# Performance work log

Hardware: AMD Instinct MI355X
Metric: run time of the kernel (lower is better)

Reference implementation:

```python
import jax, jax.numpy as jnp
import numpy as np

N = 8192          # bbox_num
C = 2048          # in_channels
IC = C // 2       # inter_channels


def setup_inputs() -> dict:
    key = jax.random.key(0)
    ks = jax.random.split(key, 12)
    s_lin = 1.0 / np.sqrt(C)    # torch Linear init scale for fan_in=C
    s_w = 1.0 / np.sqrt(IC)     # for fan_in=IC
    return {
        "x": jax.random.normal(ks[0], (N, C), dtype=jnp.float32),
        "theta_w": jax.random.uniform(ks[1], (IC, C), jnp.float32, -s_lin, s_lin),
        "theta_b": jax.random.uniform(ks[2], (IC,), jnp.float32, -s_lin, s_lin),
        "phi_w": jax.random.uniform(ks[3], (IC, C), jnp.float32, -s_lin, s_lin),
        "phi_b": jax.random.uniform(ks[4], (IC,), jnp.float32, -s_lin, s_lin),
        "g_w": jax.random.uniform(ks[5], (IC, C), jnp.float32, -s_lin, s_lin),
        "g_b": jax.random.uniform(ks[6], (IC,), jnp.float32, -s_lin, s_lin),
        "W_w": jax.random.uniform(ks[7], (C, IC), jnp.float32, -s_w, s_w),
        "W_b": jax.random.uniform(ks[8], (C,), jnp.float32, -s_w, s_w),
        "mask_w": jax.random.uniform(ks[9], (N, C), jnp.float32, -s_lin, s_lin),
        "mask_b": jax.random.uniform(ks[10], (N,), jnp.float32, -s_lin, s_lin),
    }


def reference(x, theta_w, theta_b, phi_w, phi_b, g_w, g_b, W_w, W_b, mask_w, mask_b):
    # x: [N, C]. torch Linear: y = x @ W^T + b
    g_x = x @ g_w.T + g_b              # [N, IC]
    theta_x = x @ theta_w.T + theta_b  # [N, IC]
    phi_x = x @ phi_w.T + phi_b        # [N, IC]
    f = theta_x @ phi_x.T              # [N, N]
    # resize(): ad-hoc Linear(C -> N) then softmax over last dim
    mask = jax.nn.softmax(x @ mask_w.T + mask_b, axis=-1)  # [N, N]
    f = f * mask
    f_div_C = jax.nn.softmax(f, axis=-1)  # [N, N]
    y = f_div_C @ g_x                  # [N, IC]
    W_y = y @ W_w.T + W_b              # [N, C]
    z = W_y + x                        # residual
    return (z, f_div_C)
```

## Files before the change

kernel.cpp:

```cpp
#include <hip/hip_runtime.h>
#include <hip/hip_bf16.h>

typedef __bf16 bf16_t;
typedef __bf16 bf16x8 __attribute__((ext_vector_type(8)));
typedef float f32x4 __attribute__((ext_vector_type(4)));

#define GLOAD16(gp, lp) __builtin_amdgcn_global_load_lds(                      \
    (const __attribute__((address_space(1))) void*)(gp),                       \
    (__attribute__((address_space(3))) void*)(lp), 16, 0, 0)
#define BARRIER() asm volatile("s_barrier" ::: "memory")
#define VMC(n) asm volatile("s_waitcnt vmcnt(" #n ")" ::: "memory")
#define LGK0()                                                                 \
  do {                                                                         \
    asm volatile("s_waitcnt lgkmcnt(0)" ::: "memory");                         \
    __builtin_amdgcn_sched_barrier(0);                                         \
  } while (0)

__global__ __launch_bounds__(256) void cast_f32_bf16_k(
    const float* __restrict__ in, bf16_t* __restrict__ out, long n8) {
  long i = (long)blockIdx.x * blockDim.x + threadIdx.x;
  long stride = (long)gridDim.x * blockDim.x;
  for (; i < n8; i += stride) {
    long e = i * 8;
    float4 a = *(const float4*)(in + e);
    float4 b = *(const float4*)(in + e + 4);
    bf16x8 o;
    o[0] = (__bf16)a.x; o[1] = (__bf16)a.y; o[2] = (__bf16)a.z; o[3] = (__bf16)a.w;
    o[4] = (__bf16)b.x; o[5] = (__bf16)b.y; o[6] = (__bf16)b.z; o[7] = (__bf16)b.w;
    *(bf16x8*)(out + e) = o;
  }
}

template <int BIAS, bool EMASK, bool RES, bool OUTBF16>
__global__ __launch_bounds__(512, 2) void gemm256(
    const bf16_t* __restrict__ A, long lda, const bf16_t* __restrict__ B,
    long ldb, const float* __restrict__ bias, const bf16_t* __restrict__ ml,
    const float* __restrict__ mrow, const float* __restrict__ invrow,
    const float* __restrict__ res, float* __restrict__ outf,
    bf16_t* __restrict__ outb, int M, int N, int K) {
  __shared__ __align__(1024) char lds[131072];
  const int tid = threadIdx.x;
  const int gx = N >> 8;
  int bid = blockIdx.y * gx + blockIdx.x;
  const int nwg = gridDim.x * gridDim.y;
  const int cpx = nwg >> 3;
  bid = (bid & 7) * cpx + (bid >> 3);
  const long row0 = (long)(bid / gx) * 256;
  const long col0 = (long)(bid % gx) * 256;

  const int w = tid >> 6, lane = tid & 63;
  const int wm = w >> 2, wn = w & 3;
  const int fr = lane & 15, fq = lane >> 4;

  const int arow = (wm * 128 + fr) * 128;
  const int brow = 32768 + (wn * 64 + fr) * 128;
  const int sw0 = ((fq ^ (fr & 7)) << 4);
  const int sw1 = (((4 | fq) ^ (fr & 7)) << 4);

  const int r0 = tid >> 3;
  const int s0 = (tid & 7) ^ (r0 & 7);
  const bf16_t* Ap = A + (row0 + r0) * lda + s0 * 8;
  const bf16_t* Bp = B + (col0 + r0) * ldb + s0 * 8;
  const int dstA = w * 1024;

#define STG_A(h, U)                                                            \
  {                                                                            \
    const bf16_t* s_ = Ap + (long)(h)*128 * lda + (long)(U)*64;                \
    char* d_ = lds + (((U)&1) * 65536) + (h)*16384 + dstA;                     \
    GLOAD16(s_, d_);                                                           \
    GLOAD16(s_ + 64 * lda, d_ + 8192);                                         \
  }
#define STG_B(h, U)                                                            \
  {                                                                            \
    const bf16_t* s_ = Bp + (long)(h)*128 * ldb + (long)(U)*64;                \
    char* d_ = lds + (((U)&1) * 65536) + 32768 + (h)*16384 + dstA;             \
    GLOAD16(s_, d_);                                                           \
    GLOAD16(s_ + 64 * ldb, d_ + 8192);                                         \
  }
#define RD_A(buf, s)                                                           \
  {                                                                            \
    _Pragma("unroll") for (int i = 0; i < 4; ++i) {                            \
      aS[i * 2] = *(const bf16x8*)((buf) + arow + ((s)*4 + i) * 2048 + sw0);   \
      aS[i * 2 + 1] =                                                          \
          *(const bf16x8*)((buf) + arow + ((s)*4 + i) * 2048 + sw1);           \
    }                                                                          \
  }
#define RD_B(dst, buf, s)                                                      \
  {                                                                            \
    _Pragma("unroll") for (int j = 0; j < 2; ++j) {                            \
      dst[j * 2] = *(const bf16x8*)((buf) + brow + ((s)*2 + j) * 2048 + sw0);  \
      dst[j * 2 + 1] =                                                         \
          *(const bf16x8*)((buf) + brow + ((s)*2 + j) * 2048 + sw1);           \
    }                                                                          \
  }
#define QUAD(BV, I0, J0)                                                       \
  {                                                                            \
    __builtin_amdgcn_s_setprio(1);                                             \
    _Pragma("unroll") for (int i = 0; i < 4; ++i)                              \
        _Pragma("unroll") for (int j = 0; j < 2; ++j)                          \
            _Pragma("unroll") for (int kk = 0; kk < 2; ++kk)                   \
                acc[I0 + i][J0 + j] = __builtin_amdgcn_mfma_f32_16x16x32_bf16( \
                    aS[i * 2 + kk], BV[j * 2 + kk], acc[I0 + i][J0 + j], 0, 0, \
                    0);                                                        \
    __builtin_amdgcn_s_setprio(0);                                             \
  }

  f32x4 acc[8][4] = {};
  bf16x8 aS[8], bA[4], bB[4];
  const int NT = K >> 6;

  STG_A(0, 0); STG_A(1, 0); STG_B(0, 0); STG_B(1, 0);

  for (int T = 0; T < NT; ++T) {
    char* buf = lds + (T & 1) * 65536;
    const bool ST = (T < NT - 1);
    VMC(0);
    BARRIER();
    if (ST) STG_A(0, T + 1);
    RD_A(buf, 0);
    RD_B(bA, buf, 0);
    LGK0();
    QUAD(bA, 0, 0);
    RD_B(bB, buf, 1);
    if (ST) STG_A(1, T + 1);
    LGK0();
    QUAD(bB, 0, 2);
    RD_A(buf, 1);
    if (ST) STG_B(0, T + 1);
    LGK0();
    QUAD(bB, 4, 2);
    if (ST) STG_B(1, T + 1);
    QUAD(bA, 4, 0);
  }
#undef STG_A
#undef STG_B
#undef RD_A
#undef RD_B
#undef QUAD

#pragma unroll
  for (int i = 0; i < 8; ++i)
#pragma unroll
    for (int j = 0; j < 4; ++j)
#pragma unroll
      for (int r = 0; r < 4; ++r) {
        long gi = row0 + wm * 128 + i * 16 + fq * 4 + r;
        long gj = col0 + wn * 64 + j * 16 + fr;
        float v = acc[i][j][r];
        if (BIAS == 1) v += bias[gj];
        long idx = gi * (long)N + gj;
        if (EMASK) v *= __expf((float)ml[idx] - mrow[gi]) * invrow[gi];
        if (RES) v += res[idx];
        if (OUTBF16) outb[idx] = (bf16_t)v;
        else outf[idx] = v;
      }
}

template <int BIAS, bool MUL, bool RES, bool OUTBF16, int GROUP>
__global__ __launch_bounds__(256) void gemm_nt(
    const bf16_t* __restrict__ A, const bf16_t* __restrict__ B,
    const float* __restrict__ bias, const bf16_t* __restrict__ mulm,
    const float* __restrict__ res, float* __restrict__ outf,
    bf16_t* __restrict__ outb, int M, int N, int K) {
  __shared__ bf16_t As[128 * 32];
  __shared__ bf16_t Bs[128 * 32];
  const int tid = threadIdx.x;
  const int gx = gridDim.x, gy = gridDim.y;
  const int n = blockIdx.y * gx + blockIdx.x;
  const int xcd = n & 7, q = n >> 3;
  int br, bc;
  if (GROUP == 0) { br = xcd + 8 * (q / gx); bc = q % gx; }
  else            { bc = xcd + 8 * (q / gy); br = q % gy; }
  const long row0 = (long)br * 128;
  const long col0 = (long)bc * 128;
  const int wid = tid >> 6, lane = tid & 63;
  const int wr = (wid >> 1) * 64;
  const int wc = (wid & 1) * 64;
  const int fr = lane & 15, fq = lane >> 4;
  const int sx = (fr >> 1) & 3;
  const int srow = tid >> 2;
  const int scol = ((tid & 3) ^ ((srow >> 1) & 3)) * 8;

  f32x4 acc[4][4] = {};

  const bf16_t* Ag = A + (row0 + srow) * (long)K + scol;
  const bf16_t* Bg = B + (col0 + srow) * (long)K + scol;
  const long k64 = 64L * K;
  bf16_t* ldsA = As + wid * 512;
  bf16_t* ldsB = Bs + wid * 512;

  for (int k0 = 0; k0 < K; k0 += 32) {
    GLOAD16(Ag + k0, ldsA);
    GLOAD16(Ag + k0 + k64, ldsA + 2048);
    GLOAD16(Bg + k0, ldsB);
    GLOAD16(Bg + k0 + k64, ldsB + 2048);
    __syncthreads();
    bf16x8 av[4], bv[4];
#pragma unroll
    for (int i = 0; i < 4; i++)
      av[i] = *(const bf16x8*)(As + (wr + i * 16 + fr) * 32 + ((fq ^ sx) << 3));
#pragma unroll
    for (int j = 0; j < 4; j++)
      bv[j] = *(const bf16x8*)(Bs + (wc + j * 16 + fr) * 32 + ((fq ^ sx) << 3));
#pragma unroll
    for (int i = 0; i < 4; i++)
#pragma unroll
      for (int j = 0; j < 4; j++)
        acc[i][j] = __builtin_amdgcn_mfma_f32_16x16x32_bf16(av[i], bv[j],
                                                            acc[i][j], 0, 0, 0);
    __syncthreads();
  }

#pragma unroll
  for (int i = 0; i < 4; i++) {
#pragma unroll
    for (int j = 0; j < 4; j++) {
#pragma unroll
      for (int r = 0; r < 4; r++) {
        long gi = row0 + wr + i * 16 + fq * 4 + r;
        long gj = col0 + wc + j * 16 + fr;
        float v = acc[i][j][r];
        if (BIAS == 1) v += bias[gj];
        if (BIAS == 2) v += bias[gi];
        long idx = gi * (long)N + gj;
        if (MUL) v *= (float)mulm[idx];
        if (RES) v += res[idx];
        if (OUTBF16) outb[idx] = (bf16_t)v;
        else outf[idx] = v;
      }
    }
  }
}

__global__ __launch_bounds__(256) void softmax_stats(
    const bf16_t* __restrict__ buf, float* __restrict__ mrow,
    float* __restrict__ invrow) {
  const long row = blockIdx.x;
  const bf16_t* p = buf + row * 8192;
  const int t = threadIdx.x;
  float v[32];
#pragma unroll
  for (int i = 0; i < 4; i++) {
    bf16x8 raw = *(const bf16x8*)(p + t * 32 + i * 8);
#pragma unroll
    for (int j = 0; j < 8; j++) v[i * 8 + j] = (float)raw[j];
  }
  float m = -1e30f;
#pragma unroll
  for (int i = 0; i < 32; i++) m = fmaxf(m, v[i]);
  for (int off = 32; off; off >>= 1) m = fmaxf(m, __shfl_xor(m, off, 64));
  __shared__ float redm[4], reds[4];
  if ((t & 63) == 0) redm[t >> 6] = m;
  __syncthreads();
  m = fmaxf(fmaxf(redm[0], redm[1]), fmaxf(redm[2], redm[3]));
  float s = 0.f;
#pragma unroll
  for (int i = 0; i < 32; i++) s += __expf(v[i] - m);
  for (int off = 32; off; off >>= 1) s += __shfl_xor(s, off, 64);
  if ((t & 63) == 0) reds[t >> 6] = s;
  __syncthreads();
  if (t == 0) {
    s = reds[0] + reds[1] + reds[2] + reds[3];
    mrow[row] = m;
    invrow[row] = 1.0f / s;
  }
}

__global__ __launch_bounds__(256) void softmax_f_k(bf16_t* __restrict__ fm,
                                                   float* __restrict__ outf) {
  const long row = blockIdx.x;
  bf16_t* p = fm + row * 8192;
  float* q = outf + row * 8192;
  const int t = threadIdx.x;
  float v[32];
#pragma unroll
  for (int i = 0; i < 4; i++) {
    bf16x8 raw = *(const bf16x8*)(p + t * 32 + i * 8);
#pragma unroll
    for (int j = 0; j < 8; j++) v[i * 8 + j] = (float)raw[j];
  }
  float m = -1e30f;
#pragma unroll
  for (int i = 0; i < 32; i++) m = fmaxf(m, v[i]);
  for (int off = 32; off; off >>= 1) m = fmaxf(m, __shfl_xor(m, off, 64));
  __shared__ float redm[4], reds[4];
  if ((t & 63) == 0) redm[t >> 6] = m;
  __syncthreads();
  m = fmaxf(fmaxf(redm[0], redm[1]), fmaxf(redm[2], redm[3]));
  float s = 0.f;
#pragma unroll
  for (int i = 0; i < 32; i++) {
    v[i] = __expf(v[i] - m);
    s += v[i];
  }
  for (int off = 32; off; off >>= 1) s += __shfl_xor(s, off, 64);
  if ((t & 63) == 0) reds[t >> 6] = s;
  __syncthreads();
  s = reds[0] + reds[1] + reds[2] + reds[3];
  float inv = 1.0f / s;
#pragma unroll
  for (int i = 0; i < 8; i++) {
    float4 o;
    o.x = v[i * 4 + 0] * inv;
    o.y = v[i * 4 + 1] * inv;
    o.z = v[i * 4 + 2] * inv;
    o.w = v[i * 4 + 3] * inv;
    *(float4*)(q + t * 32 + i * 4) = o;
  }
#pragma unroll
  for (int i = 0; i < 4; i++) {
    bf16x8 o;
#pragma unroll
    for (int j = 0; j < 8; j++) o[j] = (bf16_t)(v[i * 8 + j] * inv);
    *(bf16x8*)(p + t * 32 + i * 8) = o;
  }
}

extern "C" void kernel_launch(void* const* d_in, const int* in_sizes, int n_in,
                              void* d_out, int out_size, void* d_ws,
                              size_t ws_size, hipStream_t stream) {
  const int N = 8192, C = 2048, IC = 1024;
  const float* x = (const float*)d_in[0];
  const float* theta_w = (const float*)d_in[1];
  const float* theta_b = (const float*)d_in[2];
  const float* phi_w = (const float*)d_in[3];
  const float* phi_b = (const float*)d_in[4];
  const float* g_w = (const float*)d_in[5];
  const float* g_b = (const float*)d_in[6];
  const float* W_w = (const float*)d_in[7];
  const float* W_b = (const float*)d_in[8];
  const float* mask_w = (const float*)d_in[9];
  const float* mask_b = (const float*)d_in[10];

  float* z_out = (float*)d_out;
  float* f_out = z_out + (long)N * C;

  bf16_t* ML = (bf16_t*)f_out;
  bf16_t* thph16 = (bf16_t*)z_out;
  bf16_t* gT16 = thph16 + (long)N * 2048;

  char* w = (char*)d_ws;
  bf16_t* xb = (bf16_t*)w;      w += (long)N * C * 2;
  bf16_t* mwb = (bf16_t*)w;     w += (long)N * C * 2;
  bf16_t* thwb = (bf16_t*)w;    w += (long)IC * C * 2;
  bf16_t* phwb = (bf16_t*)w;    w += (long)IC * C * 2;
  bf16_t* gwb = (bf16_t*)w;     w += (long)IC * C * 2;
  bf16_t* Wwb = (bf16_t*)w;     w += (long)C * IC * 2;
  bf16_t* fm = (bf16_t*)w;      w += (long)N * N * 2;
  bf16_t* y16 = (bf16_t*)w;     w += (long)N * IC * 2;
  float* mrowb = (float*)w;     w += (long)N * 4;
  float* invrowb = (float*)w;   w += (long)N * 4;
  float* thph_b = (float*)w;    w += (long)2 * IC * 4;

  cast_f32_bf16_k<<<8192, 256, 0, stream>>>(x, xb, (long)N * C / 8);
  cast_f32_bf16_k<<<8192, 256, 0, stream>>>(mask_w, mwb, (long)N * C / 8);
  cast_f32_bf16_k<<<1024, 256, 0, stream>>>(theta_w, thwb, (long)IC * C / 8);
  cast_f32_bf16_k<<<1024, 256, 0, stream>>>(phi_w, phwb, (long)IC * C / 8);
  cast_f32_bf16_k<<<1024, 256, 0, stream>>>(g_w, gwb, (long)IC * C / 8);
  cast_f32_bf16_k<<<1024, 256, 0, stream>>>(W_w, Wwb, (long)C * IC / 8);
  hipMemcpyAsync(thph_b, theta_b, IC * 4, hipMemcpyDeviceToDevice, stream);
  hipMemcpyAsync(thph_b + IC, phi_b, IC * 4, hipMemcpyDeviceToDevice, stream);

  gemm256<1, false, false, true><<<dim3(2048 / 256, N / 256), 512, 0, stream>>>(
      xb, C, thwb, C, thph_b, nullptr, nullptr, nullptr, nullptr, nullptr,
      thph16, N, 2048, C);
  gemm_nt<2, false, false, true, 1><<<dim3(N / 128, IC / 128), 256, 0, stream>>>(
      gwb, xb, g_b, nullptr, nullptr, nullptr, gT16, IC, N, C);
  gemm256<1, false, false, true><<<dim3(N / 256, N / 256), 512, 0, stream>>>(
      xb, C, mwb, C, mask_b, nullptr, nullptr, nullptr, nullptr, nullptr,
      ML, N, N, C);
  softmax_stats<<<N, 256, 0, stream>>>(ML, mrowb, invrowb);
  gemm256<0, true, false, true><<<dim3(N / 256, N / 256), 512, 0, stream>>>(
      thph16, 2048, thph16 + 1024, 2048, nullptr, ML, mrowb, invrowb,
      nullptr, nullptr, fm, N, N, IC);
  softmax_f_k<<<N, 256, 0, stream>>>(fm, f_out);
  gemm_nt<0, false, false, true, 0><<<dim3(IC / 128, N / 128), 256, 0, stream>>>(
      fm, gT16, nullptr, nullptr, nullptr, nullptr, y16, N, IC, N);
  gemm256<1, false, true, false><<<dim3(C / 256, N / 256), 512, 0, stream>>>(
      y16, IC, Wwb, IC, W_b, nullptr, nullptr, nullptr, x, z_out, nullptr,
      N, C, IC);
}
```

Before: 1.010 ms.

## Add 256x128 LDS-pipelined GEMM for attention-times-g and fuse cast kernels

Replaces the generic 128x128 gemm_nt used for the f_div_C @ g_x product (K=8192) with a new 512-thread 256x128 tile kernel. The new kernel uses direct global-to-LDS loads, swizzled LDS reads and double buffering. It also merges the six separate f32-to-bf16 cast launches into one kernel that picks its segment by index. The goal is higher data reuse and MFMA throughput on the large-K GEMM plus fewer launches, at the cost of more LDS per block and hardcoded sizes in the cast kernel.

```diff
diff --git a/kernel.cpp b/kernel.cpp
--- a/kernel.cpp
+++ b/kernel.cpp
@@ -16,18 +16,40 @@
     __builtin_amdgcn_sched_barrier(0);                                         \
   } while (0)
 
-__global__ __launch_bounds__(256) void cast_f32_bf16_k(
-    const float* __restrict__ in, bf16_t* __restrict__ out, long n8) {
+__global__ __launch_bounds__(256) void cast_all_k(
+    const float* __restrict__ x, bf16_t* __restrict__ xb,
+    const float* __restrict__ mw, bf16_t* __restrict__ mwb,
+    const float* __restrict__ tw, bf16_t* __restrict__ twb,
+    const float* __restrict__ pw, bf16_t* __restrict__ pwb,
+    const float* __restrict__ gw, bf16_t* __restrict__ gwb,
+    const float* __restrict__ Ww, bf16_t* __restrict__ Wwb) {
+  const long NB = 2097152;
+  const long WB = 262144;
+  const long total = 2 * NB + 4 * WB;
   long i = (long)blockIdx.x * blockDim.x + threadIdx.x;
   long stride = (long)gridDim.x * blockDim.x;
-  for (; i < n8; i += stride) {
-    long e = i * 8;
-    float4 a = *(const float4*)(in + e);
-    float4 b = *(const float4*)(in + e + 4);
+  for (; i < total; i += stride) {
+    const float* src;
+    bf16_t* dst;
+    long off;
+    if (i < NB) {
+      src = x; dst = xb; off = i;
+    } else if (i < 2 * NB) {
+      src = mw; dst = mwb; off = i - NB;
+    } else {
+      long j = i - 2 * NB;
+      int seg = (int)(j >> 18);
+      off = j & (WB - 1);
+      src = (seg == 0) ? tw : (seg == 1) ? pw : (seg == 2) ? gw : Ww;
+      dst = (seg == 0) ? twb : (seg == 1) ? pwb : (seg == 2) ? gwb : Wwb;
+    }
+    long e = off * 8;
+    float4 a = *(const float4*)(src + e);
+    float4 b = *(const float4*)(src + e + 4);
     bf16x8 o;
     o[0] = (__bf16)a.x; o[1] = (__bf16)a.y; o[2] = (__bf16)a.z; o[3] = (__bf16)a.w;
     o[4] = (__bf16)b.x; o[5] = (__bf16)b.y; o[6] = (__bf16)b.z; o[7] = (__bf16)b.w;
-    *(bf16x8*)(out + e) = o;
+    *(bf16x8*)(dst + e) = o;
   }
 }
 
@@ -153,6 +175,115 @@
         if (RES) v += res[idx];
         if (OUTBF16) outb[idx] = (bf16_t)v;
         else outf[idx] = v;
+      }
+}
+
+__global__ __launch_bounds__(512, 2) void gemmT128(
+    const bf16_t* __restrict__ A, long lda, const bf16_t* __restrict__ B,
+    long ldb, bf16_t* __restrict__ out, int M, int N, int K) {
+  __shared__ __align__(1024) char lds[98304];
+  const int tid = threadIdx.x;
+  const int gx = N >> 7;
+  int bid = blockIdx.y * gx + blockIdx.x;
+  const int nwg = gridDim.x * gridDim.y;
+  const int cpx = nwg >> 3;
+  bid = (bid & 7) * cpx + (bid >> 3);
+  const long row0 = (long)(bid / gx) * 256;
+  const long col0 = (long)(bid % gx) * 128;
+
+  const int w = tid >> 6, lane = tid & 63;
+  const int wm = w >> 1, wn = w & 1;
+  const int fr = lane & 15, fq = lane >> 4;
+
+  const int arow = (wm * 64 + fr) * 128;
+  const int brow = 32768 + (wn * 64 + fr) * 128;
+  const int sw0 = ((fq ^ (fr & 7)) << 4);
+  const int sw1 = (((4 | fq) ^ (fr & 7)) << 4);
+
+  const int r0 = tid >> 3;
+  const int s0 = (tid & 7) ^ (r0 & 7);
+  const bf16_t* Ap = A + (row0 + r0) * lda + s0 * 8;
+  const bf16_t* Bp = B + (col0 + r0) * ldb + s0 * 8;
+  const int dstA = w * 1024;
+
+#define STG_A(U)                                                               \
+  {                                                                            \
+    char* d_ = lds + (((U)&1) * 49152) + dstA;                                 \
+    const bf16_t* s_ = Ap + (long)(U)*64;                                      \
+    GLOAD16(s_, d_);                                                           \
+    GLOAD16(s_ + 64 * lda, d_ + 8192);                                         \
+    GLOAD16(s_ + 128 * lda, d_ + 16384);                                       \
+    GLOAD16(s_ + 192 * lda, d_ + 24576);                                       \
+  }
+#define STG_B(U)                                                               \
+  {                                                                            \
+    char* d_ = lds + (((U)&1) * 49152) + 32768 + dstA;                         \
+    const bf16_t* s_ = Bp + (long)(U)*64;                                      \
+    GLOAD16(s_, d_);                                                           \
+    GLOAD16(s_ + 64 * ldb, d_ + 8192);                                         \
+  }
+#define RD_A(buf)                                                              \
+  {                                                                            \
+    _Pragma("unroll") for (int i = 0; i < 4; ++i) {                            \
+      aS[i * 2] = *(const bf16x8*)((buf) + arow + i * 2048 + sw0);             \
+      aS[i * 2 + 1] = *(const bf16x8*)((buf) + arow + i * 2048 + sw1);         \
+    }                                                                          \
+  }
+#define RD_B(dst, buf, s)                                                      \
+  {                                                                            \
+    _Pragma("unroll") for (int j = 0; j < 2; ++j) {                            \
+      dst[j * 2] = *(const bf16x8*)((buf) + brow + ((s)*2 + j) * 2048 + sw0);  \
+      dst[j * 2 + 1] =                                                         \
+          *(const bf16x8*)((buf) + brow + ((s)*2 + j) * 2048 + sw1);           \
+    }                                                                          \
+  }
+#define QUAD(BV, J0)                                                           \
+  {                                                                            \
+    __builtin_amdgcn_s_setprio(1);                                             \
+    _Pragma("unroll") for (int i = 0; i < 4; ++i)                              \
+        _Pragma("unroll") for (int j = 0; j < 2; ++j)                          \
+            _Pragma("unroll") for (int kk = 0; kk < 2; ++kk)                   \
+                acc[i][J0 + j] = __builtin_amdgcn_mfma_f32_16x16x32_bf16(      \
+                    aS[i * 2 + kk], BV[j * 2 + kk], acc[i][J0 + j], 0, 0, 0);  \
+    __builtin_amdgcn_s_setprio(0);                                             \
+  }
+
+  f32x4 acc[4][4] = {};
+  bf16x8 aS[8], bA[4], bB[4];
+  const int NT = K >> 6;
+
+  STG_A(0); STG_B(0);
+
+  for (int T = 0; T < NT; ++T) {
+    char* buf = lds + (T & 1) * 49152;
+    const bool ST = (T < NT - 1);
+    VMC(0);
+    BARRIER();
+    if (ST) STG_A(T + 1);
+    RD_A(buf);
+    RD_B(bA, buf, 0);
+    LGK0();
+    QUAD(bA, 0);
+    RD_B(bB, buf, 1);
+    if (ST) STG_B(T + 1);
+    LGK0();
+    QUAD(bB, 2);
+  }
+#undef STG_A
+#undef STG_B
+#undef RD_A
+#undef RD_B
+#undef QUAD
+
+#pragma unroll
+  for (int i = 0; i < 4; ++i)
+#pragma unroll
+    for (int j = 0; j < 4; ++j)
+#pragma unroll
+      for (int r = 0; r < 4; ++r) {
+        long gi = row0 + wm * 64 + i * 16 + fq * 4 + r;
+        long gj = col0 + wn * 64 + j * 16 + fr;
+        out[gi * (long)N + gj] = (bf16_t)acc[i][j][r];
       }
 }
 
@@ -352,12 +483,8 @@
   float* invrowb = (float*)w;   w += (long)N * 4;
   float* thph_b = (float*)w;    w += (long)2 * IC * 4;
 
-  cast_f32_bf16_k<<<8192, 256, 0, stream>>>(x, xb, (long)N * C / 8);
-  cast_f32_bf16_k<<<8192, 256, 0, stream>>>(mask_w, mwb, (long)N * C / 8);
-  cast_f32_bf16_k<<<1024, 256, 0, stream>>>(theta_w, thwb, (long)IC * C / 8);
-  cast_f32_bf16_k<<<1024, 256, 0, stream>>>(phi_w, phwb, (long)IC * C / 8);
-  cast_f32_bf16_k<<<1024, 256, 0, stream>>>(g_w, gwb, (long)IC * C / 8);
-  cast_f32_bf16_k<<<1024, 256, 0, stream>>>(W_w, Wwb, (long)C * IC / 8);
+  cast_all_k<<<4096, 256, 0, stream>>>(x, xb, mask_w, mwb, theta_w, thwb,
+                                       phi_w, phwb, g_w, gwb, W_w, Wwb);
   hipMemcpyAsync(thph_b, theta_b, IC * 4, hipMemcpyDeviceToDevice, stream);
   hipMemcpyAsync(thph_b + IC, phi_b, IC * 4, hipMemcpyDeviceToDevice, stream);
 
@@ -374,8 +501,8 @@
       thph16, 2048, thph16 + 1024, 2048, nullptr, ML, mrowb, invrowb,
       nullptr, nullptr, fm, N, N, IC);
   softmax_f_k<<<N, 256, 0, stream>>>(fm, f_out);
-  gemm_nt<0, false, false, true, 0><<<dim3(IC / 128, N / 128), 256, 0, stream>>>(
-      fm, gT16, nullptr, nullptr, nullptr, nullptr, y16, N, IC, N);
+  gemmT128<<<dim3(IC / 128, N / 256), 512, 0, stream>>>(
+      fm, N, gT16, N, y16, N, IC, N);
   gemm256<1, false, true, false><<<dim3(C / 256, N / 256), 512, 0, stream>>>(
       y16, IC, Wwb, IC, W_b, nullptr, nullptr, nullptr, x, z_out, nullptr,
       N, C, IC);
```

Measured after the change: 954.0 us. 5.5% less time.
